# Performance work log

Measured on AMD Instinct MI355X. Metric: run time of the kernel, lower is better.

The kernel has to match this reference:

```python
import jax, jax.numpy as jnp
import numpy as np
from jax import lax

N, L, D = 8, 2048, 512
KS = [3, 5]
DECAY = 0.2


def setup_inputs() -> dict:
    key = jax.random.key(0)
    k1, k2, k3, k4, k5 = jax.random.split(key, 5)
    return {
        "qa_embed_data": jax.random.normal(k1, (N, L, D), dtype=jnp.float32),
        "conv_w3": jax.random.normal(k2, (D, 1, KS[0]), dtype=jnp.float32) * (1.0 / KS[0]),
        "conv_w5": jax.random.normal(k3, (D, 1, KS[1]), dtype=jnp.float32) * (1.0 / KS[1]),
        "fusion_w": jax.random.normal(k4, (D, 2 * D), dtype=jnp.float32) * 0.02,
        "fusion_b": jax.random.normal(k5, (D,), dtype=jnp.float32) * 0.02,
    }


def causal_depthwise_conv(x, w, k):
    # x: [N, L, C], w: [C, 1, k] (depthwise, groups=C). Left-pad by k-1 (causal).
    xc = jnp.transpose(x, (0, 2, 1))  # [N, C, L]
    y = lax.conv_general_dilated(
        xc, w, window_strides=(1,), padding=[(k - 1, 0)],
        feature_group_count=x.shape[-1],
        dimension_numbers=("NCH", "OIH", "NCH"))
    return jnp.transpose(y, (0, 2, 1))  # [N, L, C]


def squash(v):
    norm = jnp.linalg.norm(v, axis=-1, keepdims=True)
    scale = norm ** 2 / (1.0 + norm ** 2)
    return scale * v / (norm + 1e-9)


def dynamic_routing(u, num_iterations):
    # u: [N, L, M, C]
    n, l, m, _ = u.shape
    logits = jnp.zeros((n, l, m), dtype=u.dtype)
    v = None
    for i in range(num_iterations):
        c = jax.nn.softmax(logits, axis=-1)
        s = jnp.einsum("nlm,nlmc->nlc", c, u)
        v = squash(s)
        if i < num_iterations - 1:
            logits = logits + jnp.einsum("nlmc,nlc->nlm", u, v)
    return v


def time_attention(x):
    # x: [N, L, C]; causal attention with exp(-decay*dist) bias -> add -decay*dist in log space
    l = x.shape[1]
    sim = jnp.einsum("nlc,nmc->nlm", x, x)  # [N, L, L]
    idx = jnp.arange(l)
    dist = (idx[:, None] - idx[None, :]).astype(x.dtype)  # query - key
    mask = dist >= 0  # lower-triangular causal mask
    ws = jnp.where(mask[None], sim - DECAY * dist[None], -jnp.inf)
    attn = jax.nn.softmax(ws, axis=-1)
    return jnp.einsum("nlm,nmc->nlc", attn, x)


def reference(qa_embed_data, conv_w3, conv_w5, fusion_w, fusion_b):
    trend3 = causal_depthwise_conv(qa_embed_data, conv_w3, KS[0])
    trend5 = causal_depthwise_conv(qa_embed_data, conv_w5, KS[1])
    seasonal = jnp.stack([qa_embed_data - trend3, qa_embed_data - trend5], axis=2)  # [N,L,2,C]
    trend = jnp.stack([trend3, trend5], axis=2)  # [N,L,2,C]
    seasonal_f = time_attention(dynamic_routing(seasonal, 3))
    trend_f = time_attention(dynamic_routing(trend, 3))
    cat = jnp.concatenate([seasonal_f, trend_f], axis=-1)  # [N,L,2C]
    return cat @ fusion_w.T + fusion_b
```

## Files before the change

kernel.cpp:

```cpp
#include <hip/hip_runtime.h>


typedef short     bf16x8 __attribute__((ext_vector_type(8)));
typedef float     f32x4  __attribute__((ext_vector_type(4)));
typedef unsigned short u16;
typedef u16       u16x8  __attribute__((ext_vector_type(8)));

#define NBATCH 8
#define LSEQ   2048
#define DCH    512
#define DPAD   520
#define DECAYF 0.2f
#define WTILES 6

typedef const __attribute__((address_space(1))) unsigned char* gas_t;
typedef __attribute__((address_space(3))) unsigned char* las_t;
__device__ __forceinline__ void dma16(const void* g, void* l) {
    __builtin_amdgcn_global_load_lds((gas_t)g, (las_t)l, 16, 0, 0);
}

__device__ __forceinline__ u16 f2bf(float f) {
    unsigned int u = __float_as_uint(f);
    u += 0x7fffu + ((u >> 16) & 1u);
    return (u16)(u >> 16);
}

__device__ __forceinline__ void wave_sum2(float& a, float& b) {
#pragma unroll
    for (int m = 1; m < 64; m <<= 1) {
        float ta = __shfl_xor(a, m, 64);
        float tb = __shfl_xor(b, m, 64);
        a += ta; b += tb;
    }
}
__device__ __forceinline__ void wave_sum4(float& a, float& b, float& c, float& d) {
#pragma unroll
    for (int m = 1; m < 64; m <<= 1) {
        float ta = __shfl_xor(a, m, 64);
        float tb = __shfl_xor(b, m, 64);
        float tc = __shfl_xor(c, m, 64);
        float td = __shfl_xor(d, m, 64);
        a += ta; b += tb; c += tc; d += td;
    }
}

__global__ __launch_bounds__(256) void conv_route(
    const float* __restrict__ x, const float* __restrict__ w3, const float* __restrict__ w5,
    u16* __restrict__ vs, u16* __restrict__ vt)
{
    const int wid  = threadIdx.x >> 6;
    const int lane = threadIdx.x & 63;
    const int p = blockIdx.x * 4 + wid;
    const int n = p >> 11, l = p & (LSEQ - 1);
    const int c0 = lane * 8;

    float xm[5][8];
#pragma unroll
    for (int j = 0; j < 5; ++j) {
        int ll = l - j;
        if (ll >= 0) {
            const float4* sp = (const float4*)(x + ((size_t)(n*LSEQ + ll))*DCH + c0);
            float4 a = sp[0], b = sp[1];
            xm[j][0]=a.x; xm[j][1]=a.y; xm[j][2]=a.z; xm[j][3]=a.w;
            xm[j][4]=b.x; xm[j][5]=b.y; xm[j][6]=b.z; xm[j][7]=b.w;
        } else {
#pragma unroll
            for (int i = 0; i < 8; ++i) xm[j][i] = 0.f;
        }
    }
    float f3[24], f5[40];
#pragma unroll
    for (int k = 0; k < 6; ++k)  ((float4*)f3)[k] = ((const float4*)(w3 + (size_t)c0*3))[k];
#pragma unroll
    for (int k = 0; k < 10; ++k) ((float4*)f5)[k] = ((const float4*)(w5 + (size_t)c0*5))[k];

    float t3[8], t5[8], a0[8], a1[8];
#pragma unroll
    for (int i = 0; i < 8; ++i) {
        t3[i] = f3[i*3+0]*xm[2][i] + f3[i*3+1]*xm[1][i] + f3[i*3+2]*xm[0][i];
        t5[i] = f5[i*5+0]*xm[4][i] + f5[i*5+1]*xm[3][i] + f5[i*5+2]*xm[2][i]
              + f5[i*5+3]*xm[1][i] + f5[i*5+4]*xm[0][i];
        a0[i] = xm[0][i] - t3[i];
        a1[i] = xm[0][i] - t5[i];
    }

    float ba0=0.f, ba1=0.f, bb0=0.f, bb1=0.f;
    float va[8], vb[8];
#pragma unroll
    for (int it = 0; it < 3; ++it) {
        float mxa = fmaxf(ba0, ba1), mxb = fmaxf(bb0, bb1);
        float ea0 = __expf(ba0-mxa), ea1 = __expf(ba1-mxa);
        float eb0 = __expf(bb0-mxb), eb1 = __expf(bb1-mxb);
        float ia = 1.f/(ea0+ea1), ib = 1.f/(eb0+eb1);
        float ca0 = ea0*ia, ca1 = ea1*ia, cb0 = eb0*ib, cb1 = eb1*ib;
        float na = 0.f, nb = 0.f;
        float sa[8], sb[8];
#pragma unroll
        for (int i = 0; i < 8; ++i) {
            sa[i] = ca0*a0[i] + ca1*a1[i]; na += sa[i]*sa[i];
            sb[i] = cb0*t3[i] + cb1*t5[i]; nb += sb[i]*sb[i];
        }
        wave_sum2(na, nb);
        float sca = na / ((1.f + na) * (sqrtf(na) + 1e-9f));
        float scb = nb / ((1.f + nb) * (sqrtf(nb) + 1e-9f));
#pragma unroll
        for (int i = 0; i < 8; ++i) { va[i] = sca*sa[i]; vb[i] = scb*sb[i]; }
        if (it < 2) {
            float da0=0.f, da1=0.f, db0=0.f, db1=0.f;
#pragma unroll
            for (int i = 0; i < 8; ++i) {
                da0 += a0[i]*va[i]; da1 += a1[i]*va[i];
                db0 += t3[i]*vb[i]; db1 += t5[i]*vb[i];
            }
            wave_sum4(da0, da1, db0, db1);
            ba0 += da0; ba1 += da1; bb0 += db0; bb1 += db1;
        }
    }
    u16x8 pa, pb;
#pragma unroll
    for (int i = 0; i < 8; ++i) { pa[i] = f2bf(va[i]); pb[i] = f2bf(vb[i]); }
    *(u16x8*)(vs + (size_t)p*DPAD + c0) = pa;
    *(u16x8*)(vt + (size_t)p*DPAD + c0) = pb;
}

__global__ __launch_bounds__(256) void transpose_vtile(
    const u16* __restrict__ vs, const u16* __restrict__ vt,
    u16* __restrict__ vsTt, u16* __restrict__ vtTt)
{
    __shared__ u16 T[64][65];
    const int z = blockIdx.z;
    const u16* src = ((z & 8) ? vt : vs) + (size_t)(z & 7) * LSEQ * DPAD;
    u16*       dst = ((z & 8) ? vtTt : vsTt) + (size_t)(z & 7) * 64 * DCH * 32;
    const int l0 = blockIdx.y * 64, c0 = blockIdx.x * 64;
    const int tid = threadIdx.x;
    const int rl = tid >> 3, cc = (tid & 7) * 8;
#pragma unroll
    for (int i = 0; i < 2; ++i) {
        int row = rl + i*32;
        *(u16x8*)(&T[row][cc]) = *(const u16x8*)(src + (size_t)(l0+row)*DPAD + c0 + cc);
    }
    __syncthreads();
    const int ch = tid >> 3;
    const int q3 = tid & 7;
    const int tt = q3 >> 2;
    const int sc = (q3 & 3) * 8;
#pragma unroll
    for (int i = 0; i < 2; ++i) {
        int c = ch + i*32;
        u16x8 o;
#pragma unroll
        for (int j = 0; j < 8; ++j) {
            int s = sc + j;
            int key = (s >> 1) + ((s & 1) << 4);
            o[j] = T[tt*32 + key][c];
        }
        *(u16x8*)(dst + (size_t)(blockIdx.y*2 + tt) * (DCH*32)
                      + (size_t)(c0 + c) * 32 + sc) = o;
    }
}

__global__ __launch_bounds__(256) void attn(
    const u16* __restrict__ vs, const u16* __restrict__ vt,
    const u16* __restrict__ vsTt, const u16* __restrict__ vtTt,
    u16* __restrict__ cat)
{
    __shared__ u16 Ks[33792/2];
    __shared__ u16 Vs[DCH*32];
    __shared__ unsigned int Ps32[4][16][20];

    const int inst = blockIdx.y;
    const int t = inst >> 3, n = inst & 7;
    const u16* src  = (t ? vt : vs) + (size_t)n * LSEQ * DPAD;
    const u16* srcT = (t ? vtTt : vsTt) + (size_t)n * 64 * DCH * 32;

    const int bx = blockIdx.x;
    const int r0 = (((bx & 7) << 2) | (bx >> 3)) * 64;

    const int tid  = threadIdx.x;
    const int wid  = tid >> 6, lane = tid & 63;
    const int l16  = lane & 15, quad = lane >> 4;

    bf16x8 qf[16];
    {
        const u16* qp = src + (size_t)(r0 + wid*16 + l16) * DPAD + quad*8;
#pragma unroll
        for (int kc = 0; kc < 16; ++kc) qf[kc] = *(const bf16x8*)(qp + kc*32);
    }

    f32x4 O[32];
#pragma unroll
    for (int i = 0; i < 32; ++i) O[i] = (f32x4){0.f, 0.f, 0.f, 0.f};
    f32x4 O2 = {0.f, 0.f, 0.f, 0.f};

    bf16x8 ones8;
#pragma unroll
    for (int i = 0; i < 8; ++i) ones8[i] = (short)0x3F80;

    const int kb_hi = (r0 >> 5) + 1;
    const int kb_lo = (kb_hi >= WTILES) ? kb_hi - (WTILES-1) : 0;

    {
        const u16* gK = src + (size_t)kb_lo * 32 * DPAD;
        for (int i = wid; i < 33; i += 4) dma16(gK + i*512 + lane*8, Ks + i*512);
    }

    for (int kb = kb_lo; kb <= kb_hi; ++kb) {
        __syncthreads();
        {
            const u16* gV = srcT + (size_t)kb * (DCH*32);
            for (int i = wid; i < 32; i += 4) dma16(gV + i*512 + lane*8, Vs + i*512);
        }

        f32x4 S0 = {0.f,0.f,0.f,0.f}, S1 = {0.f,0.f,0.f,0.f};
#pragma unroll
        for (int kc = 0; kc < 16; ++kc) {
            bf16x8 b0 = *(const bf16x8*)(Ks + (size_t)l16*DPAD + kc*32 + quad*8);
            bf16x8 b1 = *(const bf16x8*)(Ks + (size_t)(16+l16)*DPAD + kc*32 + quad*8);
            S0 = __builtin_amdgcn_mfma_f32_16x16x32_bf16(qf[kc], b0, S0, 0, 0, 0);
            S1 = __builtin_amdgcn_mfma_f32_16x16x32_bf16(qf[kc], b1, S1, 0, 0, 0);
        }

        const int rowg = r0 + wid*16 + quad*4;
#pragma unroll
        for (int r = 0; r < 4; ++r) {
            int row = rowg + r;
            int d0  = row - (kb*32 + l16);
            int d1  = d0 - 16;
            float p0 = (d0 >= 0) ? __expf(fmaf(-DECAYF, (float)d0, S0[r] - 1.f)) : 0.f;
            float p1 = (d1 >= 0) ? __expf(fmaf(-DECAYF, (float)d1, S1[r] - 1.f)) : 0.f;
            Ps32[wid][quad*4 + r][l16] = ((unsigned)f2bf(p1) << 16) | (unsigned)f2bf(p0);
        }

        __syncthreads();
        if (kb < kb_hi) {
            const u16* gK = src + (size_t)(kb+1) * 32 * DPAD;
            for (int i = wid; i < 33; i += 4) dma16(gK + i*512 + lane*8, Ks + i*512);
        }

        bf16x8 pf = *(const bf16x8*)(&Ps32[wid][l16][quad*4]);
#pragma unroll
        for (int ct = 0; ct < 32; ++ct) {
            bf16x8 vf = *(const bf16x8*)(Vs + (size_t)(ct*16 + l16)*32 + quad*8);
            O[ct] = __builtin_amdgcn_mfma_f32_16x16x32_bf16(pf, vf, O[ct], 0, 0, 0);
        }
        O2 = __builtin_amdgcn_mfma_f32_16x16x32_bf16(pf, ones8, O2, 0, 0, 0);
    }

    float inv[4];
#pragma unroll
    for (int r = 0; r < 4; ++r) inv[r] = 1.f / O2[r];
    const size_t rowbase = (size_t)n * LSEQ + r0 + wid*16 + quad*4;
    const int colbase = t * 512 + l16;
#pragma unroll
    for (int ct = 0; ct < 32; ++ct) {
#pragma unroll
        for (int r = 0; r < 4; ++r)
            cat[(rowbase + r) * 1024 + colbase + ct*16] = f2bf(O[ct][r] * inv[r]);
    }
}

__global__ __launch_bounds__(256) void fusion_gemm(
    const u16* __restrict__ A, const float* __restrict__ W,
    const float* __restrict__ bias, float* __restrict__ out)
{
    __shared__ u16 As[128][72];
    __shared__ u16 Bs[128][72];
    const int m0 = blockIdx.x * 128;
    const int n0 = blockIdx.y * 128;
    const int tid = threadIdx.x;
    const int wid = tid >> 6, lane = tid & 63;
    const int l16 = lane & 15, quad = lane >> 4;
    const int wm = (wid >> 1) * 64, wn = (wid & 1) * 64;

    f32x4 acc[4][4];
#pragma unroll
    for (int i = 0; i < 4; ++i)
#pragma unroll
        for (int j = 0; j < 4; ++j) acc[i][j] = (f32x4){0.f, 0.f, 0.f, 0.f};

    for (int kb = 0; kb < 16; ++kb) {
#pragma unroll
        for (int i = 0; i < 4; ++i) {
            int id = tid + i*256;
            int row = id >> 3, kc = id & 7;
            *(u16x8*)(&As[row][kc*8]) = *(const u16x8*)(A + (size_t)(m0+row)*1024 + kb*64 + kc*8);
            const float4* wp = (const float4*)(W + (size_t)(n0+row)*1024 + kb*64 + kc*8);
            float4 wa = wp[0], wb4 = wp[1];
            u16x8 bb;
            bb[0]=f2bf(wa.x); bb[1]=f2bf(wa.y); bb[2]=f2bf(wa.z); bb[3]=f2bf(wa.w);
            bb[4]=f2bf(wb4.x); bb[5]=f2bf(wb4.y); bb[6]=f2bf(wb4.z); bb[7]=f2bf(wb4.w);
            *(u16x8*)(&Bs[row][kc*8]) = bb;
        }
        __syncthreads();
#pragma unroll
        for (int k2 = 0; k2 < 2; ++k2) {
            bf16x8 af[4], bfr[4];
#pragma unroll
            for (int i = 0; i < 4; ++i) {
                af[i]  = *(const bf16x8*)(&As[wm + i*16 + l16][k2*32 + quad*8]);
                bfr[i] = *(const bf16x8*)(&Bs[wn + i*16 + l16][k2*32 + quad*8]);
            }
#pragma unroll
            for (int i = 0; i < 4; ++i)
#pragma unroll
                for (int j = 0; j < 4; ++j)
                    acc[i][j] = __builtin_amdgcn_mfma_f32_16x16x32_bf16(af[i], bfr[j], acc[i][j], 0, 0, 0);
        }
        __syncthreads();
    }
#pragma unroll
    for (int j = 0; j < 4; ++j) {
        int col = n0 + wn + j*16 + l16;
        float bv = bias[col];
#pragma unroll
        for (int i = 0; i < 4; ++i) {
            int rowb = m0 + wm + i*16 + quad*4;
#pragma unroll
            for (int r = 0; r < 4; ++r)
                out[(size_t)(rowb + r)*512 + col] = acc[i][j][r] + bv;
        }
    }
}

extern "C" void kernel_launch(void* const* d_in, const int* in_sizes, int n_in,
                              void* d_out, int out_size, void* d_ws, size_t ws_size,
                              hipStream_t stream)
{
    (void)in_sizes; (void)n_in; (void)out_size; (void)ws_size;
    const float* x  = (const float*)d_in[0];
    const float* w3 = (const float*)d_in[1];
    const float* w5 = (const float*)d_in[2];
    const float* fw = (const float*)d_in[3];
    const float* fb = (const float*)d_in[4];
    float* out = (float*)d_out;

    const size_t SZP = (size_t)NBATCH * LSEQ * DPAD;
    const size_t SZT = (size_t)NBATCH * 64 * DCH * 32;
    u16* vs   = (u16*)d_ws;
    u16* vt   = vs   + SZP;
    u16* vsTt = vt   + SZP;
    u16* vtTt = vsTt + SZT;
    u16* cat  = vtTt + SZT;

    conv_route    <<<4096, 256, 0, stream>>>(x, w3, w5, vs, vt);
    transpose_vtile<<<dim3(8, 32, 16), 256, 0, stream>>>(vs, vt, vsTt, vtTt);
    attn          <<<dim3(32, 16), 256, 0, stream>>>(vs, vt, vsTt, vtTt, cat);
    fusion_gemm   <<<dim3(128, 4), 256, 0, stream>>>(cat, fw, fb, out);
}
```

Measured before the change: 200.2 us.

## Shrink attention key window, use Gram-matrix routing, split MFMA accumulator chains

The dynamic-routing loop now computes the per-position Gram entries (a0·a0, a0·a1, a1·a1 and the trend equivalents) once with a single six-way wave reduction. Each routing iteration then derives the squash norm and the logit updates in closed form, replacing four wave-wide shuffle reductions per iteration. The attention window shrinks from 6 to 4 key tiles of 32, relying on the exp(-0.2·dist) decay and the bounded squashed norms so that dropped keys contribute negligibly. The QK MFMA chain is split into two independent accumulators to shorten the dependency chain. Risks are slightly different rounding in the routing, and a truncation error from the narrower window that remains tiny given the decay.

```diff
diff --git a/kernel.cpp b/kernel.cpp
--- a/kernel.cpp
+++ b/kernel.cpp
@@ -11,7 +11,7 @@
 #define DCH    512
 #define DPAD   520
 #define DECAYF 0.2f
-#define WTILES 6
+#define WTILES 4
 
 typedef const __attribute__((address_space(1))) unsigned char* gas_t;
 typedef __attribute__((address_space(3))) unsigned char* las_t;
@@ -25,22 +25,17 @@
     return (u16)(u >> 16);
 }
 
-__device__ __forceinline__ void wave_sum2(float& a, float& b) {
-#pragma unroll
-    for (int m = 1; m < 64; m <<= 1) {
-        float ta = __shfl_xor(a, m, 64);
-        float tb = __shfl_xor(b, m, 64);
-        a += ta; b += tb;
-    }
-}
-__device__ __forceinline__ void wave_sum4(float& a, float& b, float& c, float& d) {
+__device__ __forceinline__ void wave_sum6(float& a, float& b, float& c,
+                                          float& d, float& e, float& f) {
 #pragma unroll
     for (int m = 1; m < 64; m <<= 1) {
         float ta = __shfl_xor(a, m, 64);
         float tb = __shfl_xor(b, m, 64);
         float tc = __shfl_xor(c, m, 64);
         float td = __shfl_xor(d, m, 64);
-        a += ta; b += tb; c += tc; d += td;
+        float te = __shfl_xor(e, m, 64);
+        float tf = __shfl_xor(f, m, 64);
+        a += ta; b += tb; c += tc; d += td; e += te; f += tf;
     }
 }
 
@@ -84,41 +79,40 @@
         a1[i] = xm[0][i] - t5[i];
     }
 
+    float A1=0.f, B1=0.f, C1=0.f, A2=0.f, B2=0.f, C2=0.f;
+#pragma unroll
+    for (int i = 0; i < 8; ++i) {
+        A1 += a0[i]*a0[i]; B1 += a0[i]*a1[i]; C1 += a1[i]*a1[i];
+        A2 += t3[i]*t3[i]; B2 += t3[i]*t5[i]; C2 += t5[i]*t5[i];
+    }
+    wave_sum6(A1, B1, C1, A2, B2, C2);
+
     float ba0=0.f, ba1=0.f, bb0=0.f, bb1=0.f;
-    float va[8], vb[8];
+    float ca0=0.5f, ca1=0.5f, sca=0.f, cb0=0.5f, cb1=0.5f, scb=0.f;
 #pragma unroll
     for (int it = 0; it < 3; ++it) {
         float mxa = fmaxf(ba0, ba1), mxb = fmaxf(bb0, bb1);
         float ea0 = __expf(ba0-mxa), ea1 = __expf(ba1-mxa);
         float eb0 = __expf(bb0-mxb), eb1 = __expf(bb1-mxb);
         float ia = 1.f/(ea0+ea1), ib = 1.f/(eb0+eb1);
-        float ca0 = ea0*ia, ca1 = ea1*ia, cb0 = eb0*ib, cb1 = eb1*ib;
-        float na = 0.f, nb = 0.f;
-        float sa[8], sb[8];
-#pragma unroll
-        for (int i = 0; i < 8; ++i) {
-            sa[i] = ca0*a0[i] + ca1*a1[i]; na += sa[i]*sa[i];
-            sb[i] = cb0*t3[i] + cb1*t5[i]; nb += sb[i]*sb[i];
-        }
-        wave_sum2(na, nb);
-        float sca = na / ((1.f + na) * (sqrtf(na) + 1e-9f));
-        float scb = nb / ((1.f + nb) * (sqrtf(nb) + 1e-9f));
-#pragma unroll
-        for (int i = 0; i < 8; ++i) { va[i] = sca*sa[i]; vb[i] = scb*sb[i]; }
+        ca0 = ea0*ia; ca1 = ea1*ia; cb0 = eb0*ib; cb1 = eb1*ib;
+        float na = ca0*ca0*A1 + 2.f*ca0*ca1*B1 + ca1*ca1*C1;
+        float nb = cb0*cb0*A2 + 2.f*cb0*cb1*B2 + cb1*cb1*C2;
+        sca = na / ((1.f + na) * (sqrtf(na) + 1e-9f));
+        scb = nb / ((1.f + nb) * (sqrtf(nb) + 1e-9f));
         if (it < 2) {
-            float da0=0.f, da1=0.f, db0=0.f, db1=0.f;
-#pragma unroll
-            for (int i = 0; i < 8; ++i) {
-                da0 += a0[i]*va[i]; da1 += a1[i]*va[i];
-                db0 += t3[i]*vb[i]; db1 += t5[i]*vb[i];
-            }
-            wave_sum4(da0, da1, db0, db1);
-            ba0 += da0; ba1 += da1; bb0 += db0; bb1 += db1;
+            ba0 += sca*(ca0*A1 + ca1*B1);
+            ba1 += sca*(ca0*B1 + ca1*C1);
+            bb0 += scb*(cb0*A2 + cb1*B2);
+            bb1 += scb*(cb0*B2 + cb1*C2);
         }
     }
     u16x8 pa, pb;
 #pragma unroll
-    for (int i = 0; i < 8; ++i) { pa[i] = f2bf(va[i]); pb[i] = f2bf(vb[i]); }
+    for (int i = 0; i < 8; ++i) {
+        pa[i] = f2bf(sca*(ca0*a0[i] + ca1*a1[i]));
+        pb[i] = f2bf(scb*(cb0*t3[i] + cb1*t5[i]));
+    }
     *(u16x8*)(vs + (size_t)p*DPAD + c0) = pa;
     *(u16x8*)(vt + (size_t)p*DPAD + c0) = pb;
 }
@@ -211,14 +205,23 @@
             for (int i = wid; i < 32; i += 4) dma16(gV + i*512 + lane*8, Vs + i*512);
         }
 
-        f32x4 S0 = {0.f,0.f,0.f,0.f}, S1 = {0.f,0.f,0.f,0.f};
-#pragma unroll
-        for (int kc = 0; kc < 16; ++kc) {
+        f32x4 S0a = {0.f,0.f,0.f,0.f}, S1a = {0.f,0.f,0.f,0.f};
+        f32x4 S0b = {0.f,0.f,0.f,0.f}, S1b = {0.f,0.f,0.f,0.f};
+#pragma unroll
+        for (int kc = 0; kc < 8; ++kc) {
             bf16x8 b0 = *(const bf16x8*)(Ks + (size_t)l16*DPAD + kc*32 + quad*8);
             bf16x8 b1 = *(const bf16x8*)(Ks + (size_t)(16+l16)*DPAD + kc*32 + quad*8);
-            S0 = __builtin_amdgcn_mfma_f32_16x16x32_bf16(qf[kc], b0, S0, 0, 0, 0);
-            S1 = __builtin_amdgcn_mfma_f32_16x16x32_bf16(qf[kc], b1, S1, 0, 0, 0);
-        }
+            S0a = __builtin_amdgcn_mfma_f32_16x16x32_bf16(qf[kc], b0, S0a, 0, 0, 0);
+            S1a = __builtin_amdgcn_mfma_f32_16x16x32_bf16(qf[kc], b1, S1a, 0, 0, 0);
+        }
+#pragma unroll
+        for (int kc = 8; kc < 16; ++kc) {
+            bf16x8 b0 = *(const bf16x8*)(Ks + (size_t)l16*DPAD + kc*32 + quad*8);
+            bf16x8 b1 = *(const bf16x8*)(Ks + (size_t)(16+l16)*DPAD + kc*32 + quad*8);
+            S0b = __builtin_amdgcn_mfma_f32_16x16x32_bf16(qf[kc], b0, S0b, 0, 0, 0);
+            S1b = __builtin_amdgcn_mfma_f32_16x16x32_bf16(qf[kc], b1, S1b, 0, 0, 0);
+        }
+        f32x4 S0 = S0a + S0b, S1 = S1a + S1b;
 
         const int rowg = r0 + wid*16 + quad*4;
 #pragma unroll
```

New measurement: 193.1 us. -3.5%, faster.
